# Kernel tuning notes

Measured on AMD Instinct MI355X. Metric: run time of the kernel, lower is better.

## Reference

```python
import jax, jax.numpy as jnp
import numpy as np


def _gcn_conv(x, src, dst, W, b, num_nodes, deg_inv_sqrt):
    # PyG GCNConv: h = x @ W, then normalized scatter-add over edges (incl. self loops), + bias
    h = x @ W  # [N, d_out]
    norm = deg_inv_sqrt[src] * deg_inv_sqrt[dst]  # [E']
    msg = h[src] * norm[:, None]  # gather + scale, [E', d_out]
    out = jax.ops.segment_sum(msg, dst, num_segments=num_nodes)  # scatter-add to targets
    return out + b


def reference(x, edge_index, W1, b1, W2, b2, num_nodes):
    src0, dst0 = edge_index[0], edge_index[1]
    loop = jnp.arange(num_nodes, dtype=edge_index.dtype)
    # add self loops (PyG default add_self_loops=True)
    src = jnp.concatenate([src0, loop])
    dst = jnp.concatenate([dst0, loop])
    # symmetric normalization D^{-1/2} (A+I) D^{-1/2}, degree from self-looped graph
    deg = jax.ops.segment_sum(jnp.ones_like(src, dtype=x.dtype), dst, num_segments=num_nodes)
    deg_inv_sqrt = jnp.where(deg > 0, jax.lax.rsqrt(jnp.maximum(deg, 1)), 0.0).astype(x.dtype)

    z = jax.nn.relu(_gcn_conv(x, src, dst, W1, b1, num_nodes, deg_inv_sqrt))
    z = jax.nn.relu(_gcn_conv(z, src, dst, W2, b2, num_nodes, deg_inv_sqrt))
    return z


def setup_inputs() -> dict:
    key = jax.random.key(0)
    k1, k2, k3, k4 = jax.random.split(key, 4)
    N, E, D, H = 50000, 1600000, 128, 128
    x = jax.random.normal(k1, (N, D), dtype=jnp.float32)
    edge_index = jax.random.randint(k2, (2, E), 0, N, dtype=jnp.int64)
    s = 1.0 / np.sqrt(D)
    W1 = jax.random.normal(k3, (D, H), dtype=jnp.float32) * s
    W2 = jax.random.normal(k4, (H, H), dtype=jnp.float32) * s
    return {
        "x": x,
        "edge_index": edge_index,
        "W1": W1,
        "b1": jnp.zeros((H,), jnp.float32),
        "W2": W2,
        "b2": jnp.zeros((H,), jnp.float32),
        "num_nodes": N,
    }
```

## Files before the change

kernel.cpp:

```cpp
#include <hip/hip_runtime.h>

#define FD 128
#define BSH 7
#define CH 2048
#define CHT 8
#define KMAX 512
#define SCAP 8192
#define NCH 8
#define CSH 13
#define NPW 7

typedef __attribute__((ext_vector_type(8))) short bf16x8;
typedef __attribute__((ext_vector_type(4))) float f32x4;

__device__ inline unsigned bfr(float f) {
    unsigned u = __float_as_uint(f);
    return (u + 0x7FFF + ((u >> 16) & 1)) >> 16;
}
__device__ inline float uplo(unsigned p) { return __uint_as_float(p << 16); }
__device__ inline float uphi(unsigned p) { return __uint_as_float(p & 0xFFFF0000u); }


__global__ __launch_bounds__(256) void partition_kernel(
        const int* __restrict__ src, const int* __restrict__ dst,
        int* __restrict__ lstartG, int* __restrict__ total,
        int* __restrict__ pairs, int E, int K) {
    __shared__ int lcnt[KMAX];
    __shared__ int lstart[KMAX];
    __shared__ int sm[256];
    __shared__ int staged[CH];
    int t = threadIdx.x;
    int base = blockIdx.x * CH;
    int n = min(CH, E - base);

    lcnt[t] = 0; lcnt[t + 256] = 0;
    __syncthreads();

    int pk[CHT]; int bn[CHT];
    #pragma unroll
    for (int j = 0; j < CHT; ++j) {
        int i = t + j * 256;
        bn[j] = -1;
        if (i < n) {
            int d = dst[base + i];
            int s = src[base + i];
            bn[j] = d >> BSH;
            pk[j] = ((d & ((1 << BSH) - 1)) << 17) | s;
            atomicAdd(&lcnt[bn[j]], 1);
        }
    }
    __syncthreads();

    int c0 = lcnt[2 * t], c1 = lcnt[2 * t + 1];
    int s2 = c0 + c1;
    sm[t] = s2;
    __syncthreads();
    for (int off = 1; off < 256; off <<= 1) {
        int add = (t >= off) ? sm[t - off] : 0;
        __syncthreads();
        sm[t] += add;
        __syncthreads();
    }
    int ex = sm[t] - s2;
    lstart[2 * t] = ex;     lstart[2 * t + 1] = ex + c0;
    lcnt[2 * t]   = ex;     lcnt[2 * t + 1]   = ex + c0;
    __syncthreads();

    #pragma unroll
    for (int j = 0; j < CHT; ++j) {
        if (bn[j] >= 0) {
            int pos = atomicAdd(&lcnt[bn[j]], 1);
            staged[pos] = pk[j];
        }
    }
    __syncthreads();

    for (int i = t; i < n; i += 256)
        pairs[base + i] = staged[i];

    size_t lrow = (size_t)blockIdx.x * (K + 1);
    for (int b = t; b < K; b += 256) {
        lstartG[lrow + b] = lstart[b];
        int c = lcnt[b] - lstart[b];
        if (c) atomicAdd(&total[b], c);
    }
    if (t == 0) lstartG[lrow + K] = n;
}

__global__ __launch_bounds__(512) void totscan_kernel(
        const int* __restrict__ total, int* __restrict__ bbase,
        int* __restrict__ rp, int K, int E, int N) {
    __shared__ int sm[512];
    int t = threadIdx.x;
    int v = (t < K) ? total[t] : 0;
    sm[t] = v;
    __syncthreads();
    for (int off = 1; off < 512; off <<= 1) {
        int add = (t >= off) ? sm[t - off] : 0;
        __syncthreads();
        sm[t] += add;
        __syncthreads();
    }
    if (t < K) bbase[t] = sm[t] - v;
    if (t == 0) { bbase[K] = E; rp[N] = E; }
}

__global__ __launch_bounds__(256) void tr_kernel(
        const int* __restrict__ A, int* __restrict__ B, int R, int C) {
    __shared__ int tile[32][33];
    int c0 = blockIdx.x * 32, r0 = blockIdx.y * 32;
    int tx = threadIdx.x, ty = threadIdx.y;
    for (int i = ty; i < 32; i += 8) {
        int r = r0 + i, c = c0 + tx;
        if (r < R && c < C) tile[i][tx] = A[(size_t)r * C + c];
    }
    __syncthreads();
    for (int i = ty; i < 32; i += 8) {
        int c = c0 + i, r = r0 + tx;
        if (c < C && r < R) B[(size_t)c * R + r] = tile[tx][i];
    }
}

__global__ __launch_bounds__(256) void build_kernel(
        const int* __restrict__ pairs, const int* __restrict__ lstartT,
        const int* __restrict__ bbase, int* __restrict__ rp,
        int* __restrict__ rpc, float* __restrict__ dis,
        int* __restrict__ col, int N, int PB, int K) {
    __shared__ int staged[SCAP];
    __shared__ int lcnt[128 * NCH];
    __shared__ int pref[128 * NCH];
    __shared__ int sm[256];
    int b = blockIdx.x;
    int t = threadIdx.x;
    int nbase = b << BSH;
    int nn = min(1 << BSH, N - nbase);
    int beg = bbase[b];
    int cnt = bbase[b + 1] - beg;

    int fp[4], fl0[4], flen[4];
    int nf = 0, mysum = 0;
    for (int p = t; p < PB; p += 256) {
        int l0 = lstartT[(size_t)b * PB + p];
        int l1 = lstartT[(size_t)(b + 1) * PB + p];
        fp[nf] = p; fl0[nf] = l0; flen[nf] = l1 - l0;
        mysum += l1 - l0;
        ++nf;
    }
    sm[t] = mysum;
    __syncthreads();
    for (int off = 1; off < 256; off <<= 1) {
        int add = (t >= off) ? sm[t - off] : 0;
        __syncthreads();
        sm[t] += add;
        __syncthreads();
    }
    int o = sm[t] - mysum;

    lcnt[t] = 0; lcnt[t + 256] = 0; lcnt[t + 512] = 0; lcnt[t + 768] = 0;

    if (cnt <= SCAP) {
        for (int f = 0; f < nf; ++f) {
            int gbase = fp[f] * CH + fl0[f];
            for (int i = 0; i < flen[f]; ++i) staged[o + i] = pairs[gbase + i];
            o += flen[f];
        }
        __syncthreads();
        for (int i = t; i < cnt; i += 256) {
            int p = staged[i];
            atomicAdd(&lcnt[((p >> 17) << 3) | ((p & 0x1FFFF) >> CSH)], 1);
        }
    } else {
        __syncthreads();
        for (int f = 0; f < nf; ++f) {
            int gbase = fp[f] * CH + fl0[f];
            for (int i = 0; i < flen[f]; ++i) {
                int p = pairs[gbase + i];
                atomicAdd(&lcnt[((p >> 17) << 3) | ((p & 0x1FFFF) >> CSH)], 1);
            }
        }
    }
    __syncthreads();

    int b0 = 4 * t;
    int c0 = lcnt[b0], c1 = lcnt[b0 + 1], c2 = lcnt[b0 + 2], c3 = lcnt[b0 + 3];
    int s4 = c0 + c1 + c2 + c3;
    sm[t] = s4;
    __syncthreads();
    for (int off = 1; off < 256; off <<= 1) {
        int add = (t >= off) ? sm[t - off] : 0;
        __syncthreads();
        sm[t] += add;
        __syncthreads();
    }
    int ex = sm[t] - s4;
    pref[b0] = ex; pref[b0 + 1] = ex + c0;
    pref[b0 + 2] = ex + c0 + c1; pref[b0 + 3] = ex + c0 + c1 + c2;
    __syncthreads();

    if (t < 128 && t < nn) {
        int rs = pref[t << 3];
        int re = (t < 127) ? pref[(t + 1) << 3] : cnt;
        rp[nbase + t] = beg + rs;
        dis[nbase + t] = rsqrtf((float)(re - rs + 1));
    }
    #pragma unroll
    for (int j = 0; j < 4; ++j) {
        int bin = b0 + j;
        int row = bin >> 3, p = bin & (NCH - 1);
        if (row < nn) rpc[(size_t)p * N + nbase + row] = beg + pref[bin];
    }
    __syncthreads();
    lcnt[b0]     = beg + pref[b0];
    lcnt[b0 + 1] = beg + pref[b0 + 1];
    lcnt[b0 + 2] = beg + pref[b0 + 2];
    lcnt[b0 + 3] = beg + pref[b0 + 3];
    __syncthreads();

    if (cnt <= SCAP) {
        for (int i = t; i < cnt; i += 256) {
            int p = staged[i];
            int key = ((p >> 17) << 3) | ((p & 0x1FFFF) >> CSH);
            int pos = atomicAdd(&lcnt[key], 1);
            col[pos] = p & 0x1FFFF;
        }
    } else {
        for (int f = 0; f < nf; ++f) {
            int gbase = fp[f] * CH + fl0[f];
            for (int i = 0; i < flen[f]; ++i) {
                int p = pairs[gbase + i];
                int key = ((p >> 17) << 3) | ((p & 0x1FFFF) >> CSH);
                int pos = atomicAdd(&lcnt[key], 1);
                col[pos] = p & 0x1FFFF;
            }
        }
    }
}


__global__ void wt_kernel(const float* __restrict__ W1, unsigned short* __restrict__ W1T,
                          const float* __restrict__ W2, unsigned short* __restrict__ W2T) {
    int k = blockIdx.x & (FD - 1);
    int n = threadIdx.x;
    if (blockIdx.x < FD) W1T[n * FD + k] = (unsigned short)bfr(W1[k * FD + n]);
    else                 W2T[n * FD + k] = (unsigned short)bfr(W2[k * FD + n]);
}


#define APAD 8
#define ASTR (FD + APAD)

template <bool A32>
__device__ void gemm_body(const void* __restrict__ Ap,
                          const unsigned short* __restrict__ WT,
                          const float* __restrict__ dis,
                          unsigned short* __restrict__ C, int M) {
    __shared__ unsigned short As[128 * ASTR];
    __shared__ unsigned short Bs[128 * ASTR];
    int tid = threadIdx.x;
    int lane = tid & 63;
    int wave = tid >> 6;
    int quad = lane >> 4;
    int l16 = lane & 15;
    int rowBase = blockIdx.x * 128;

    #pragma unroll
    for (int p = 0; p < 8; ++p) {
        int r = p * 16 + (tid >> 4);
        int cq = (tid & 15) * 8;
        int gr = rowBase + r;
        uint4 v = make_uint4(0u, 0u, 0u, 0u);
        if (A32) {
            if (gr < M) {
                const float* a = (const float*)Ap + (size_t)gr * FD + cq;
                float4 f0 = *(const float4*)a;
                float4 f1 = *(const float4*)(a + 4);
                v.x = bfr(f0.x) | (bfr(f0.y) << 16);
                v.y = bfr(f0.z) | (bfr(f0.w) << 16);
                v.z = bfr(f1.x) | (bfr(f1.y) << 16);
                v.w = bfr(f1.z) | (bfr(f1.w) << 16);
            }
        } else {
            if (gr < M) v = *(const uint4*)((const unsigned short*)Ap + (size_t)gr * FD + cq);
        }
        *(uint4*)&As[r * ASTR + cq] = v;
        *(uint4*)&Bs[r * ASTR + cq] = *(const uint4*)&WT[(size_t)r * FD + cq];
    }
    __syncthreads();

    int m0 = wave * 32;
    f32x4 acc[2][8] = {};
    #pragma unroll
    for (int kt = 0; kt < 4; ++kt) {
        int ko = kt * 32 + quad * 8;
        bf16x8 a0 = *(bf16x8*)&As[(m0 + l16) * ASTR + ko];
        bf16x8 a1 = *(bf16x8*)&As[(m0 + 16 + l16) * ASTR + ko];
        #pragma unroll
        for (int n = 0; n < 8; ++n) {
            bf16x8 b = *(bf16x8*)&Bs[(n * 16 + l16) * ASTR + ko];
            acc[0][n] = __builtin_amdgcn_mfma_f32_16x16x32_bf16(a0, b, acc[0][n], 0, 0, 0);
            acc[1][n] = __builtin_amdgcn_mfma_f32_16x16x32_bf16(a1, b, acc[1][n], 0, 0, 0);
        }
    }

    #pragma unroll
    for (int ms = 0; ms < 2; ++ms) {
        #pragma unroll
        for (int r = 0; r < 4; ++r) {
            int grow = rowBase + m0 + ms * 16 + quad * 4 + r;
            if (grow < M) {
                float dv = dis[grow];
                #pragma unroll
                for (int n = 0; n < 8; ++n) {
                    C[(size_t)grow * FD + n * 16 + l16] =
                        (unsigned short)bfr(dv * acc[ms][n][r]);
                }
            }
        }
    }
}

__global__ __launch_bounds__(256) void gemm_mfma_f32(
        const float* __restrict__ A, const unsigned short* __restrict__ WT,
        const float* __restrict__ dis, unsigned short* __restrict__ C, int M) {
    gemm_body<true>(A, WT, dis, C, M);
}

__global__ __launch_bounds__(256) void gemm_mfma_bf16(
        const unsigned short* __restrict__ A, const unsigned short* __restrict__ WT,
        const float* __restrict__ dis, unsigned short* __restrict__ C, int M) {
    gemm_body<false>(A, WT, dis, C, M);
}


__global__ __launch_bounds__(256, 7) void agg_kernel(
        const unsigned* __restrict__ h, const float* __restrict__ dis,
        const int* __restrict__ rpc, const int* __restrict__ col,
        const float2* __restrict__ bias, void* __restrict__ out, int N, int obf) {
    int wid = __builtin_amdgcn_readfirstlane(blockIdx.x * 4 + threadIdx.y);
    int t = threadIdx.x;
    int v0 = wid * NPW;
    if (v0 >= N) return;
    int nv = min(NPW, N - v0);

    float2 acc[NPW];
    #pragma unroll
    for (int s = 0; s < NPW; ++s) acc[s] = make_float2(0.0f, 0.0f);

    for (int p = 0; p < NCH - 1; ++p) {
        int st[NPW], en[NPW];
        #pragma unroll
        for (int s = 0; s < NPW; ++s) {
            if (s < nv) {
                st[s] = rpc[(size_t)p * N + v0 + s];
                en[s] = rpc[(size_t)(p + 1) * N + v0 + s];
            } else { st[s] = 0; en[s] = 0; }
        }
        #pragma unroll
        for (int s = 0; s < NPW; ++s) {
            int e = st[s], end = en[s];
            for (; e + 4 <= end; e += 4) {
                int u0 = col[e], u1 = col[e + 1], u2 = col[e + 2], u3 = col[e + 3];
                unsigned q0 = h[(size_t)u0 * 64 + t];
                unsigned q1 = h[(size_t)u1 * 64 + t];
                unsigned q2 = h[(size_t)u2 * 64 + t];
                unsigned q3 = h[(size_t)u3 * 64 + t];
                acc[s].x += uplo(q0); acc[s].y += uphi(q0);
                acc[s].x += uplo(q1); acc[s].y += uphi(q1);
                acc[s].x += uplo(q2); acc[s].y += uphi(q2);
                acc[s].x += uplo(q3); acc[s].y += uphi(q3);
            }
            for (; e < end; ++e) {
                unsigned q = h[(size_t)col[e] * 64 + t];
                acc[s].x += uplo(q); acc[s].y += uphi(q);
            }
        }
    }

    float2 bb = bias[t];
    #pragma unroll
    for (int s = 0; s < NPW; ++s) {
        if (s < nv) {
            int v = v0 + s;
            float dv = dis[v];
            size_t vb = (size_t)v * 64 + t;
            unsigned hp = h[vb];
            float rx = fmaxf(fmaf(dv, acc[s].x + uplo(hp), bb.x), 0.0f);
            float ry = fmaxf(fmaf(dv, acc[s].y + uphi(hp), bb.y), 0.0f);
            if (obf) ((unsigned*)out)[vb] = bfr(rx) | (bfr(ry) << 16);
            else     ((float2*)out)[vb] = make_float2(rx, ry);
        }
    }
}


extern "C" void kernel_launch(void* const* d_in, const int* in_sizes, int n_in,
                              void* d_out, int out_size, void* d_ws, size_t ws_size,
                              hipStream_t stream) {
    const float* x  = (const float*)d_in[0];
    const int*   ei = (const int*)d_in[1];
    const float* W1 = (const float*)d_in[2];
    const float* b1 = (const float*)d_in[3];
    const float* W2 = (const float*)d_in[4];
    const float* b2 = (const float*)d_in[5];

    int N = in_sizes[0] / FD;
    int E = in_sizes[1] / 2;
    const int* src = ei;
    const int* dst = ei + E;
    int K = (N + (1 << BSH) - 1) >> BSH;
    int PB = (E + CH - 1) / CH;

    char* base = (char*)d_ws;
    size_t off = 0;
    auto align256 = [](size_t v) { return (v + 255) & ~(size_t)255; };
    int*            rp    = (int*)(base + off);            off += align256((size_t)(N + 1) * 4);
    float*          dis   = (float*)(base + off);          off += align256((size_t)N * 4);
    int*            total = (int*)(base + off);            off += align256(512 * 4);
    int*            bbase = (int*)(base + off);            off += align256(513 * 4);
    unsigned short* w1t   = (unsigned short*)(base + off); off += align256((size_t)FD * FD * 2);
    unsigned short* w2t   = (unsigned short*)(base + off); off += align256((size_t)FD * FD * 2);
    int*            col   = (int*)(base + off);            off += align256((size_t)E * 4);
    unsigned short* hbuf  = (unsigned short*)(base + off); off += align256((size_t)N * FD * 2);
    unsigned short* z1    = (unsigned short*)(base + off); off += align256((size_t)N * FD * 2);
    int*            pairs = (int*)(base + off);            off += align256((size_t)E * 4);
    int*            rpc   = (int*)(base + off);            off += align256((size_t)NCH * N * 4);
    int*            lstartG = (int*)hbuf;
    int*            lstartT = (int*)z1;
    (void)ws_size; (void)n_in; (void)out_size;

    (void)hipMemsetAsync(total, 0, 512 * 4, stream);
    partition_kernel<<<PB, 256, 0, stream>>>(src, dst, lstartG, total, pairs, E, K);
    totscan_kernel  <<<1, 512, 0, stream>>>(total, bbase, rp, K, E, N);
    dim3 trb(32, 8);
    dim3 trg((K + 1 + 31) / 32, (PB + 31) / 32);
    tr_kernel       <<<trg, trb, 0, stream>>>(lstartG, lstartT, PB, K + 1);
    build_kernel    <<<K, 256, 0, stream>>>(pairs, lstartT, bbase, rp, rpc, dis, col, N, PB, K);

    wt_kernel<<<2 * FD, FD, 0, stream>>>(W1, w1t, W2, w2t);

    dim3 aggBlk(64, 4);
    int aggGrid = (N + 4 * NPW - 1) / (4 * NPW);
    int gemmGrid = (N + 127) / 128;

    gemm_mfma_f32 <<<gemmGrid, 256, 0, stream>>>(x, w1t, dis, hbuf, N);
    agg_kernel<<<aggGrid, aggBlk, 0, stream>>>((const unsigned*)hbuf, dis, rpc, col,
                                               (const float2*)b1, z1, N, 1);
    gemm_mfma_bf16<<<gemmGrid, 256, 0, stream>>>(z1, w2t, dis, hbuf, N);
    agg_kernel<<<aggGrid, aggBlk, 0, stream>>>((const unsigned*)hbuf, dis, rpc, col,
                                               (const float2*)b2, d_out, N, 0);
}
```

Baseline: 297.9 us.

## Group CSR by 8-node groups per column chunk with packed row selectors

Result: slower. 652.2 us (+118.9%).

```diff
diff --git a/kernel.cpp b/kernel.cpp
--- a/kernel.cpp
+++ b/kernel.cpp
@@ -8,7 +8,7 @@
 #define SCAP 8192
 #define NCH 8
 #define CSH 13
-#define NPW 7
+#define NPW 8
 
 typedef __attribute__((ext_vector_type(8))) short bf16x8;
 typedef __attribute__((ext_vector_type(4))) float f32x4;
@@ -88,8 +88,7 @@
 }
 
 __global__ __launch_bounds__(512) void totscan_kernel(
-        const int* __restrict__ total, int* __restrict__ bbase,
-        int* __restrict__ rp, int K, int E, int N) {
+        const int* __restrict__ total, int* __restrict__ bbase, int K, int E) {
     __shared__ int sm[512];
     int t = threadIdx.x;
     int v = (t < K) ? total[t] : 0;
@@ -102,7 +101,7 @@
         __syncthreads();
     }
     if (t < K) bbase[t] = sm[t] - v;
-    if (t == 0) { bbase[K] = E; rp[N] = E; }
+    if (t == 0) bbase[K] = E;
 }
 
 __global__ __launch_bounds__(256) void tr_kernel(
@@ -123,12 +122,12 @@
 
 __global__ __launch_bounds__(256) void build_kernel(
         const int* __restrict__ pairs, const int* __restrict__ lstartT,
-        const int* __restrict__ bbase, int* __restrict__ rp,
-        int* __restrict__ rpc, float* __restrict__ dis,
-        int* __restrict__ col, int N, int PB, int K) {
+        const int* __restrict__ bbase, int* __restrict__ rs,
+        float* __restrict__ dis, int* __restrict__ col,
+        int N, int PB, int K, int NG) {
     __shared__ int staged[SCAP];
-    __shared__ int lcnt[128 * NCH];
-    __shared__ int pref[128 * NCH];
+    __shared__ int lcnt[1024];
+    __shared__ int pref[1024];
     __shared__ int sm[256];
     int b = blockIdx.x;
     int t = threadIdx.x;
@@ -167,7 +166,7 @@
         __syncthreads();
         for (int i = t; i < cnt; i += 256) {
             int p = staged[i];
-            atomicAdd(&lcnt[((p >> 17) << 3) | ((p & 0x1FFFF) >> CSH)], 1);
+            atomicAdd(&lcnt[(((p & 0x1FFFF) >> CSH) << 7) | (p >> 17)], 1);
         }
     } else {
         __syncthreads();
@@ -175,7 +174,7 @@
             int gbase = fp[f] * CH + fl0[f];
             for (int i = 0; i < flen[f]; ++i) {
                 int p = pairs[gbase + i];
-                atomicAdd(&lcnt[((p >> 17) << 3) | ((p & 0x1FFFF) >> CSH)], 1);
+                atomicAdd(&lcnt[(((p & 0x1FFFF) >> CSH) << 7) | (p >> 17)], 1);
             }
         }
     }
@@ -197,17 +196,18 @@
     pref[b0 + 2] = ex + c0 + c1; pref[b0 + 3] = ex + c0 + c1 + c2;
     __syncthreads();
 
-    if (t < 128 && t < nn) {
-        int rs = pref[t << 3];
-        int re = (t < 127) ? pref[(t + 1) << 3] : cnt;
-        rp[nbase + t] = beg + rs;
-        dis[nbase + t] = rsqrtf((float)(re - rs + 1));
+    if (t < 128) {
+        int deg = 0;
+        #pragma unroll
+        for (int pp = 0; pp < 8; ++pp) deg += lcnt[(pp << 7) | t];
+        if (t < nn) dis[nbase + t] = rsqrtf((float)(deg + 1));
     }
     #pragma unroll
     for (int j = 0; j < 4; ++j) {
         int bin = b0 + j;
-        int row = bin >> 3, p = bin & (NCH - 1);
-        if (row < nn) rpc[(size_t)p * N + nbase + row] = beg + pref[bin];
+        if ((bin & 7) == 0)
+            rs[(size_t)(bin >> 7) * NG + (b << 4) + ((bin & 127) >> 3)] =
+                beg + pref[bin];
     }
     __syncthreads();
     lcnt[b0]     = beg + pref[b0];
@@ -219,18 +219,18 @@
     if (cnt <= SCAP) {
         for (int i = t; i < cnt; i += 256) {
             int p = staged[i];
-            int key = ((p >> 17) << 3) | ((p & 0x1FFFF) >> CSH);
+            int key = (((p & 0x1FFFF) >> CSH) << 7) | (p >> 17);
             int pos = atomicAdd(&lcnt[key], 1);
-            col[pos] = p & 0x1FFFF;
+            col[pos] = (((p >> 17) & 7) << 17) | (p & 0x1FFFF);
         }
     } else {
         for (int f = 0; f < nf; ++f) {
             int gbase = fp[f] * CH + fl0[f];
             for (int i = 0; i < flen[f]; ++i) {
                 int p = pairs[gbase + i];
-                int key = ((p >> 17) << 3) | ((p & 0x1FFFF) >> CSH);
+                int key = (((p & 0x1FFFF) >> CSH) << 7) | (p >> 17);
                 int pos = atomicAdd(&lcnt[key], 1);
-                col[pos] = p & 0x1FFFF;
+                col[pos] = (((p >> 17) & 7) << 17) | (p & 0x1FFFF);
             }
         }
     }
@@ -332,60 +332,73 @@
 }
 
 
-__global__ __launch_bounds__(256, 7) void agg_kernel(
+__global__ __launch_bounds__(256, 6) void agg_kernel(
         const unsigned* __restrict__ h, const float* __restrict__ dis,
-        const int* __restrict__ rpc, const int* __restrict__ col,
-        const float2* __restrict__ bias, void* __restrict__ out, int N, int obf) {
-    int wid = __builtin_amdgcn_readfirstlane(blockIdx.x * 4 + threadIdx.y);
+        const int* __restrict__ rs, const int* __restrict__ col,
+        const float2* __restrict__ bias, void* __restrict__ out,
+        int N, int NG, int obf) {
+    __shared__ float accs[4][NPW][64][2];
+    int w = threadIdx.y;
     int t = threadIdx.x;
-    int v0 = wid * NPW;
-    if (v0 >= N) return;
-    int nv = min(NPW, N - v0);
-
-    float2 acc[NPW];
-    #pragma unroll
-    for (int s = 0; s < NPW; ++s) acc[s] = make_float2(0.0f, 0.0f);
+    int gg = __builtin_amdgcn_readfirstlane(blockIdx.x * 4 + w);
+    if (gg >= NG) return;
+    int v0 = gg * NPW;
+
+    #pragma unroll
+    for (int sN = 0; sN < NPW; ++sN) {
+        accs[w][sN][t][0] = 0.0f;
+        accs[w][sN][t][1] = 0.0f;
+    }
+
+    float2 racc = make_float2(0.0f, 0.0f);
+    int cursel = 0;
 
     for (int p = 0; p < NCH - 1; ++p) {
-        int st[NPW], en[NPW];
-        #pragma unroll
-        for (int s = 0; s < NPW; ++s) {
-            if (s < nv) {
-                st[s] = rpc[(size_t)p * N + v0 + s];
-                en[s] = rpc[(size_t)(p + 1) * N + v0 + s];
-            } else { st[s] = 0; en[s] = 0; }
-        }
-        #pragma unroll
-        for (int s = 0; s < NPW; ++s) {
-            int e = st[s], end = en[s];
-            for (; e + 4 <= end; e += 4) {
-                int u0 = col[e], u1 = col[e + 1], u2 = col[e + 2], u3 = col[e + 3];
-                unsigned q0 = h[(size_t)u0 * 64 + t];
-                unsigned q1 = h[(size_t)u1 * 64 + t];
-                unsigned q2 = h[(size_t)u2 * 64 + t];
-                unsigned q3 = h[(size_t)u3 * 64 + t];
-                acc[s].x += uplo(q0); acc[s].y += uphi(q0);
-                acc[s].x += uplo(q1); acc[s].y += uphi(q1);
-                acc[s].x += uplo(q2); acc[s].y += uphi(q2);
-                acc[s].x += uplo(q3); acc[s].y += uphi(q3);
-            }
-            for (; e < end; ++e) {
-                unsigned q = h[(size_t)col[e] * 64 + t];
-                acc[s].x += uplo(q); acc[s].y += uphi(q);
-            }
-        }
-    }
+        int s = __builtin_amdgcn_readfirstlane(rs[(size_t)p * NG + gg]);
+        int e2 = __builtin_amdgcn_readfirstlane(
+            ((gg & 15) == 15) ? rs[(size_t)(p + 1) * NG + gg - 15]
+                              : rs[(size_t)p * NG + gg + 1]);
+        while (s < e2) {
+            int c[16]; unsigned q[16];
+            #pragma unroll
+            for (int i = 0; i < 16; ++i) {
+                if (s + i < e2) {
+                    c[i] = col[s + i];
+                    q[i] = h[(size_t)(c[i] & 0x1FFFF) * 64 + t];
+                }
+            }
+            #pragma unroll
+            for (int i = 0; i < 16; ++i) {
+                if (s + i < e2) {
+                    int sel = __builtin_amdgcn_readfirstlane(c[i]) >> 17;
+                    if (sel != cursel) {
+                        atomicAdd(&accs[w][cursel][t][0], racc.x);
+                        atomicAdd(&accs[w][cursel][t][1], racc.y);
+                        racc.x = 0.0f; racc.y = 0.0f;
+                        cursel = sel;
+                    }
+                    racc.x += uplo(q[i]);
+                    racc.y += uphi(q[i]);
+                }
+            }
+            s += 16;
+        }
+    }
+    atomicAdd(&accs[w][cursel][t][0], racc.x);
+    atomicAdd(&accs[w][cursel][t][1], racc.y);
 
     float2 bb = bias[t];
     #pragma unroll
-    for (int s = 0; s < NPW; ++s) {
-        if (s < nv) {
-            int v = v0 + s;
-            float dv = dis[v];
+    for (int sN = 0; sN < NPW; ++sN) {
+        int v = v0 + sN;
+        if (v < N) {
+            float ax = accs[w][sN][t][0];
+            float ay = accs[w][sN][t][1];
             size_t vb = (size_t)v * 64 + t;
             unsigned hp = h[vb];
-            float rx = fmaxf(fmaf(dv, acc[s].x + uplo(hp), bb.x), 0.0f);
-            float ry = fmaxf(fmaf(dv, acc[s].y + uphi(hp), bb.y), 0.0f);
+            float dv = dis[v];
+            float rx = fmaxf(fmaf(dv, ax + uplo(hp), bb.x), 0.0f);
+            float ry = fmaxf(fmaf(dv, ay + uphi(hp), bb.y), 0.0f);
             if (obf) ((unsigned*)out)[vb] = bfr(rx) | (bfr(ry) << 16);
             else     ((float2*)out)[vb] = make_float2(rx, ry);
         }
@@ -409,11 +422,11 @@
     const int* dst = ei + E;
     int K = (N + (1 << BSH) - 1) >> BSH;
     int PB = (E + CH - 1) / CH;
+    int NG = K << 4;
 
     char* base = (char*)d_ws;
     size_t off = 0;
     auto align256 = [](size_t v) { return (v + 255) & ~(size_t)255; };
-    int*            rp    = (int*)(base + off);            off += align256((size_t)(N + 1) * 4);
     float*          dis   = (float*)(base + off);          off += align256((size_t)N * 4);
     int*            total = (int*)(base + off);            off += align256(512 * 4);
     int*            bbase = (int*)(base + off);            off += align256(513 * 4);
@@ -423,29 +436,29 @@
     unsigned short* hbuf  = (unsigned short*)(base + off); off += align256((size_t)N * FD * 2);
     unsigned short* z1    = (unsigned short*)(base + off); off += align256((size_t)N * FD * 2);
     int*            pairs = (int*)(base + off);            off += align256((size_t)E * 4);
-    int*            rpc   = (int*)(base + off);            off += align256((size_t)NCH * N * 4);
+    int*            rs    = (int*)(base + off);            off += align256((size_t)NCH * NG * 4);
     int*            lstartG = (int*)hbuf;
     int*            lstartT = (int*)z1;
     (void)ws_size; (void)n_in; (void)out_size;
 
     (void)hipMemsetAsync(total, 0, 512 * 4, stream);
     partition_kernel<<<PB, 256, 0, stream>>>(src, dst, lstartG, total, pairs, E, K);
-    totscan_kernel  <<<1, 512, 0, stream>>>(total, bbase, rp, K, E, N);
+    totscan_kernel  <<<1, 512, 0, stream>>>(total, bbase, K, E);
     dim3 trb(32, 8);
     dim3 trg((K + 1 + 31) / 32, (PB + 31) / 32);
     tr_kernel       <<<trg, trb, 0, stream>>>(lstartG, lstartT, PB, K + 1);
-    build_kernel    <<<K, 256, 0, stream>>>(pairs, lstartT, bbase, rp, rpc, dis, col, N, PB, K);
+    build_kernel    <<<K, 256, 0, stream>>>(pairs, lstartT, bbase, rs, dis, col, N, PB, K, NG);
 
     wt_kernel<<<2 * FD, FD, 0, stream>>>(W1, w1t, W2, w2t);
 
     dim3 aggBlk(64, 4);
-    int aggGrid = (N + 4 * NPW - 1) / (4 * NPW);
+    int aggGrid = (NG + 3) / 4;
     int gemmGrid = (N + 127) / 128;
 
     gemm_mfma_f32 <<<gemmGrid, 256, 0, stream>>>(x, w1t, dis, hbuf, N);
-    agg_kernel<<<aggGrid, aggBlk, 0, stream>>>((const unsigned*)hbuf, dis, rpc, col,
-                                               (const float2*)b1, z1, N, 1);
+    agg_kernel<<<aggGrid, aggBlk, 0, stream>>>((const unsigned*)hbuf, dis, rs, col,
+                                               (const float2*)b1, z1, N, NG, 1);
     gemm_mfma_bf16<<<gemmGrid, 256, 0, stream>>>(z1, w2t, dis, hbuf, N);
-    agg_kernel<<<aggGrid, aggBlk, 0, stream>>>((const unsigned*)hbuf, dis, rpc, col,
-                                               (const float2*)b2, d_out, N, 0);
-}
+    agg_kernel<<<aggGrid, aggBlk, 0, stream>>>((const unsigned*)hbuf, dis, rs, col,
+                                               (const float2*)b2, d_out, N, NG, 0);
+}
```

## Interleave edge gathers across sixteen nodes per wave in aggregation

Applied to the files above, without the earlier changes.

Result: slower. 455.9 us (+53.1%).

```diff
diff --git a/kernel.cpp b/kernel.cpp
--- a/kernel.cpp
+++ b/kernel.cpp
@@ -8,7 +8,7 @@
 #define SCAP 8192
 #define NCH 8
 #define CSH 13
-#define NPW 7
+#define NPW 16
 
 typedef __attribute__((ext_vector_type(8))) short bf16x8;
 typedef __attribute__((ext_vector_type(4))) float f32x4;
@@ -88,8 +88,7 @@
 }
 
 __global__ __launch_bounds__(512) void totscan_kernel(
-        const int* __restrict__ total, int* __restrict__ bbase,
-        int* __restrict__ rp, int K, int E, int N) {
+        const int* __restrict__ total, int* __restrict__ bbase, int K, int E) {
     __shared__ int sm[512];
     int t = threadIdx.x;
     int v = (t < K) ? total[t] : 0;
@@ -102,7 +101,7 @@
         __syncthreads();
     }
     if (t < K) bbase[t] = sm[t] - v;
-    if (t == 0) { bbase[K] = E; rp[N] = E; }
+    if (t == 0) bbase[K] = E;
 }
 
 __global__ __launch_bounds__(256) void tr_kernel(
@@ -123,9 +122,9 @@
 
 __global__ __launch_bounds__(256) void build_kernel(
         const int* __restrict__ pairs, const int* __restrict__ lstartT,
-        const int* __restrict__ bbase, int* __restrict__ rp,
-        int* __restrict__ rpc, float* __restrict__ dis,
-        int* __restrict__ col, int N, int PB, int K) {
+        const int* __restrict__ bbase, int* __restrict__ rpc,
+        float* __restrict__ dis, int* __restrict__ col,
+        int N, int PB, int K) {
     __shared__ int staged[SCAP];
     __shared__ int lcnt[128 * NCH];
     __shared__ int pref[128 * NCH];
@@ -200,7 +199,6 @@
     if (t < 128 && t < nn) {
         int rs = pref[t << 3];
         int re = (t < 127) ? pref[(t + 1) << 3] : cnt;
-        rp[nbase + t] = beg + rs;
         dis[nbase + t] = rsqrtf((float)(re - rs + 1));
     }
     #pragma unroll
@@ -332,55 +330,56 @@
 }
 
 
-__global__ __launch_bounds__(256, 7) void agg_kernel(
+__global__ __launch_bounds__(256) void agg_kernel(
         const unsigned* __restrict__ h, const float* __restrict__ dis,
         const int* __restrict__ rpc, const int* __restrict__ col,
-        const float2* __restrict__ bias, void* __restrict__ out, int N, int obf) {
-    int wid = __builtin_amdgcn_readfirstlane(blockIdx.x * 4 + threadIdx.y);
+        const float2* __restrict__ bias, void* __restrict__ out,
+        int N, int E, int obf) {
+    int gg = __builtin_amdgcn_readfirstlane(blockIdx.x * 4 + threadIdx.y);
     int t = threadIdx.x;
-    int v0 = wid * NPW;
+    int v0 = gg * NPW;
     if (v0 >= N) return;
-    int nv = min(NPW, N - v0);
 
     float2 acc[NPW];
     #pragma unroll
     for (int s = 0; s < NPW; ++s) acc[s] = make_float2(0.0f, 0.0f);
 
     for (int p = 0; p < NCH - 1; ++p) {
-        int st[NPW], en[NPW];
+        int st[NPW], len[NPW];
+        int maxlen = 0;
         #pragma unroll
         for (int s = 0; s < NPW; ++s) {
-            if (s < nv) {
-                st[s] = rpc[(size_t)p * N + v0 + s];
-                en[s] = rpc[(size_t)(p + 1) * N + v0 + s];
-            } else { st[s] = 0; en[s] = 0; }
-        }
-        #pragma unroll
-        for (int s = 0; s < NPW; ++s) {
-            int e = st[s], end = en[s];
-            for (; e + 4 <= end; e += 4) {
-                int u0 = col[e], u1 = col[e + 1], u2 = col[e + 2], u3 = col[e + 3];
-                unsigned q0 = h[(size_t)u0 * 64 + t];
-                unsigned q1 = h[(size_t)u1 * 64 + t];
-                unsigned q2 = h[(size_t)u2 * 64 + t];
-                unsigned q3 = h[(size_t)u3 * 64 + t];
-                acc[s].x += uplo(q0); acc[s].y += uphi(q0);
-                acc[s].x += uplo(q1); acc[s].y += uphi(q1);
-                acc[s].x += uplo(q2); acc[s].y += uphi(q2);
-                acc[s].x += uplo(q3); acc[s].y += uphi(q3);
-            }
-            for (; e < end; ++e) {
-                unsigned q = h[(size_t)col[e] * 64 + t];
-                acc[s].x += uplo(q); acc[s].y += uphi(q);
-            }
+            int vv = min(v0 + s, N - 1);
+            st[s] = __builtin_amdgcn_readfirstlane(rpc[(size_t)p * N + vv]);
+            int en = __builtin_amdgcn_readfirstlane(rpc[(size_t)(p + 1) * N + vv]);
+            len[s] = en - st[s];
+            maxlen = max(maxlen, len[s]);
+        }
+        maxlen = min(maxlen, 4096);
+
+        for (int j = 0; j < maxlen; ++j) {
+            int u[NPW];
+            #pragma unroll
+            for (int s = 0; s < NPW; ++s)
+                u[s] = col[min(st[s] + j, E - 1)];
+            unsigned q[NPW];
+            #pragma unroll
+            for (int s = 0; s < NPW; ++s)
+                if (j < len[s]) q[s] = h[(size_t)u[s] * 64 + t];
+            #pragma unroll
+            for (int s = 0; s < NPW; ++s)
+                if (j < len[s]) {
+                    acc[s].x += uplo(q[s]);
+                    acc[s].y += uphi(q[s]);
+                }
         }
     }
 
     float2 bb = bias[t];
     #pragma unroll
     for (int s = 0; s < NPW; ++s) {
-        if (s < nv) {
-            int v = v0 + s;
+        int v = v0 + s;
+        if (v < N) {
             float dv = dis[v];
             size_t vb = (size_t)v * 64 + t;
             unsigned hp = h[vb];
@@ -413,7 +412,6 @@
     char* base = (char*)d_ws;
     size_t off = 0;
     auto align256 = [](size_t v) { return (v + 255) & ~(size_t)255; };
-    int*            rp    = (int*)(base + off);            off += align256((size_t)(N + 1) * 4);
     float*          dis   = (float*)(base + off);          off += align256((size_t)N * 4);
     int*            total = (int*)(base + off);            off += align256(512 * 4);
     int*            bbase = (int*)(base + off);            off += align256(513 * 4);
@@ -430,22 +428,23 @@
 
     (void)hipMemsetAsync(total, 0, 512 * 4, stream);
     partition_kernel<<<PB, 256, 0, stream>>>(src, dst, lstartG, total, pairs, E, K);
-    totscan_kernel  <<<1, 512, 0, stream>>>(total, bbase, rp, K, E, N);
+    totscan_kernel  <<<1, 512, 0, stream>>>(total, bbase, K, E);
     dim3 trb(32, 8);
     dim3 trg((K + 1 + 31) / 32, (PB + 31) / 32);
     tr_kernel       <<<trg, trb, 0, stream>>>(lstartG, lstartT, PB, K + 1);
-    build_kernel    <<<K, 256, 0, stream>>>(pairs, lstartT, bbase, rp, rpc, dis, col, N, PB, K);
+    build_kernel    <<<K, 256, 0, stream>>>(pairs, lstartT, bbase, rpc, dis, col, N, PB, K);
 
     wt_kernel<<<2 * FD, FD, 0, stream>>>(W1, w1t, W2, w2t);
 
     dim3 aggBlk(64, 4);
-    int aggGrid = (N + 4 * NPW - 1) / (4 * NPW);
+    int nGroups = (N + NPW - 1) / NPW;
+    int aggGrid = (nGroups + 3) / 4;
     int gemmGrid = (N + 127) / 128;
 
     gemm_mfma_f32 <<<gemmGrid, 256, 0, stream>>>(x, w1t, dis, hbuf, N);
     agg_kernel<<<aggGrid, aggBlk, 0, stream>>>((const unsigned*)hbuf, dis, rpc, col,
-                                               (const float2*)b1, z1, N, 1);
+                                               (const float2*)b1, z1, N, E, 1);
     gemm_mfma_bf16<<<gemmGrid, 256, 0, stream>>>(z1, w2t, dis, hbuf, N);
     agg_kernel<<<aggGrid, aggBlk, 0, stream>>>((const unsigned*)hbuf, dis, rpc, col,
-                                               (const float2*)b2, d_out, N, 0);
-}
+                                               (const float2*)b2, d_out, N, E, 0);
+}
```
